# Optimization experiments

Hardware: AMD Instinct MI355X
Metric: run time of the kernel (lower is better)

## Reference

```python
import jax, jax.numpy as jnp
import numpy as np

B, H, W = 32, 480, 640
EPS = 1e-4


def _se3_exp(xi):
    """xi: [B,6] twist (v, w) -> (t [B,3], q [B,4] xyzw) of exp(xi)."""
    v, w = xi[:, :3], xi[:, 3:]
    theta2 = jnp.sum(w * w, axis=-1, keepdims=True)           # [B,1]
    theta = jnp.sqrt(theta2)
    small = theta < EPS
    safe_t = jnp.where(small, 1.0, theta)
    safe_t2 = jnp.where(small, 1.0, theta2)
    # quaternion: [sin(theta/2)/theta * w, cos(theta/2)], Taylor for small theta
    s_over = jnp.where(small, 0.5 - theta2 / 48.0, jnp.sin(0.5 * theta) / safe_t)
    q = jnp.concatenate([s_over * w, jnp.cos(0.5 * theta)], axis=-1)  # [B,4]
    # left Jacobian V = I + Bc*hat(w) + Cc*hat(w)^2
    Bc = jnp.where(small, 0.5 - theta2 / 24.0, (1.0 - jnp.cos(theta)) / safe_t2)
    Cc = jnp.where(small, 1.0 / 6.0 - theta2 / 120.0,
                   (theta - jnp.sin(theta)) / (safe_t2 * safe_t))
    wxv = jnp.cross(w, v)
    t = v + Bc * wxv + Cc * jnp.cross(w, wxv)                 # [B,3]
    return t, q


def _qmul(q1, q2):
    """Hamilton product, xyzw convention."""
    x1, y1, z1, w1 = jnp.split(q1, 4, axis=-1)
    x2, y2, z2, w2 = jnp.split(q2, 4, axis=-1)
    return jnp.concatenate([
        w1 * x2 + x1 * w2 + y1 * z2 - z1 * y2,
        w1 * y2 - x1 * z2 + y1 * w2 + z1 * x2,
        w1 * z2 + x1 * y2 - y1 * x2 + z1 * w2,
        w1 * w2 - x1 * x2 - y1 * y2 - z1 * z2,
    ], axis=-1)


def _qrot(q, v):
    """Rotate vectors v [B,3] by unit quaternions q [B,4] (xyzw)."""
    u, w = q[:, :3], q[:, 3:]
    uv = jnp.cross(u, v)
    return v + 2.0 * (w * uv + jnp.cross(u, uv))


def setup_inputs() -> dict:
    key = jax.random.key(0)
    ks = jax.random.split(key, 6)
    cp = jax.random.normal(ks[0], (B, 7), jnp.float32)
    qn = cp[:, 3:] / jnp.linalg.norm(cp[:, 3:], axis=-1, keepdims=True)
    curr_pose = jnp.concatenate([cp[:, :3], qn], axis=-1)
    curr_depth = 0.5 + 9.5 * jax.random.uniform(ks[1], (B, H, W), jnp.float32)
    delta_pose = 0.01 * jax.random.normal(ks[2], (B, 6), jnp.float32)
    delta_depth = jax.random.normal(ks[3], (B, H, W), jnp.float32)
    a_p = jax.random.uniform(ks[4], (B, 1), jnp.float32)
    a_d = jax.random.uniform(ks[5], (B, H, W), jnp.float32)
    return {"curr_pose": curr_pose, "curr_depth": curr_depth,
            "delta_pose": delta_pose, "delta_depth": delta_depth,
            "a_p": a_p, "a_d": a_d}


def reference(curr_pose, curr_depth, delta_pose, delta_depth, a_p, a_d):
    new_depth = jnp.maximum(curr_depth + a_d * delta_depth, 0.1)
    t_d, q_d = _se3_exp(a_p * delta_pose)
    t_c, q_c = curr_pose[:, :3], curr_pose[:, 3:]
    # compose: new_pose = delta_SE3 * curr_pose
    t_new = _qrot(q_d, t_c) + t_d
    q_new = _qmul(q_d, q_c)
    new_pose = jnp.concatenate([t_new, q_new], axis=-1)
    return (new_pose, new_depth)
```

## Files before the change

kernel.cpp:

```cpp
#include <hip/hip_runtime.h>
#include <math.h>

#define SE3_EPS 1e-4f

__global__ __launch_bounds__(256) void PoseDepthUpdater_fused_kernel(
    const float* __restrict__ curr_pose,
    const float* __restrict__ curr_depth,
    const float* __restrict__ delta_pose,
    const float* __restrict__ delta_depth,
    const float* __restrict__ a_p,
    const float* __restrict__ a_d,
    float* __restrict__ out_pose,
    float* __restrict__ out_depth,
    int Bn, long n)
{
    if (blockIdx.x == 0 && threadIdx.x < (unsigned)Bn) {
        int b = threadIdx.x;
        float ap = a_p[b];
        float v0 = ap * delta_pose[b*6+0];
        float v1 = ap * delta_pose[b*6+1];
        float v2 = ap * delta_pose[b*6+2];
        float w0 = ap * delta_pose[b*6+3];
        float w1 = ap * delta_pose[b*6+4];
        float w2 = ap * delta_pose[b*6+5];

        float theta2 = w0*w0 + w1*w1 + w2*w2;
        float theta  = sqrtf(theta2);
        bool  small  = theta < SE3_EPS;
        float safe_t  = small ? 1.0f : theta;
        float safe_t2 = small ? 1.0f : theta2;

        float s_over = small ? (0.5f - theta2 * (1.0f/48.0f))
                             : (sinf(0.5f*theta) / safe_t);
        float qx = s_over * w0, qy = s_over * w1, qz = s_over * w2;
        float qw = cosf(0.5f * theta);

        float Bc = small ? (0.5f - theta2 * (1.0f/24.0f))
                         : ((1.0f - cosf(theta)) / safe_t2);
        float Cc = small ? (1.0f/6.0f - theta2 * (1.0f/120.0f))
                         : ((theta - sinf(theta)) / (safe_t2 * safe_t));

        float cx = w1*v2 - w2*v1;
        float cy = w2*v0 - w0*v2;
        float cz = w0*v1 - w1*v0;
        float dx = w1*cz - w2*cy;
        float dy = w2*cx - w0*cz;
        float dz = w0*cy - w1*cx;

        float td0 = v0 + Bc*cx + Cc*dx;
        float td1 = v1 + Bc*cy + Cc*dy;
        float td2 = v2 + Bc*cz + Cc*dz;

        float tc0 = curr_pose[b*7+0], tc1 = curr_pose[b*7+1], tc2 = curr_pose[b*7+2];
        float qcx = curr_pose[b*7+3], qcy = curr_pose[b*7+4];
        float qcz = curr_pose[b*7+5], qcw = curr_pose[b*7+6];

        float uvx = qy*tc2 - qz*tc1;
        float uvy = qz*tc0 - qx*tc2;
        float uvz = qx*tc1 - qy*tc0;
        float uuvx = qy*uvz - qz*uvy;
        float uuvy = qz*uvx - qx*uvz;
        float uuvz = qx*uvy - qy*uvx;

        float tn0 = tc0 + 2.0f*(qw*uvx + uuvx) + td0;
        float tn1 = tc1 + 2.0f*(qw*uvy + uuvy) + td1;
        float tn2 = tc2 + 2.0f*(qw*uvz + uuvz) + td2;

        float nx = qw*qcx + qx*qcw + qy*qcz - qz*qcy;
        float ny = qw*qcy - qx*qcz + qy*qcw + qz*qcx;
        float nz = qw*qcz + qx*qcy - qy*qcx + qz*qcw;
        float nw = qw*qcw - qx*qcx - qy*qcy - qz*qcz;

        out_pose[b*7+0] = tn0;
        out_pose[b*7+1] = tn1;
        out_pose[b*7+2] = tn2;
        out_pose[b*7+3] = nx;
        out_pose[b*7+4] = ny;
        out_pose[b*7+5] = nz;
        out_pose[b*7+6] = nw;
    }

    long n4 = n >> 2;
    const float4* __restrict__ c4 = (const float4*)curr_depth;
    const float4* __restrict__ d4 = (const float4*)delta_depth;
    const float4* __restrict__ a4 = (const float4*)a_d;
    float4* __restrict__ o4 = (float4*)out_depth;

    long tid    = (long)blockIdx.x * blockDim.x + threadIdx.x;
    long stride = (long)gridDim.x * blockDim.x;

    for (long i = tid; i < n4; i += stride) {
        float4 c = c4[i];
        float4 d = d4[i];
        float4 a = a4[i];
        float4 r;
        r.x = fmaxf(fmaf(a.x, d.x, c.x), 0.1f);
        r.y = fmaxf(fmaf(a.y, d.y, c.y), 0.1f);
        r.z = fmaxf(fmaf(a.z, d.z, c.z), 0.1f);
        r.w = fmaxf(fmaf(a.w, d.w, c.w), 0.1f);
        o4[i] = r;
    }

    long tail_start = n4 << 2;
    for (long j = tail_start + tid; j < n; j += stride) {
        out_depth[j] = fmaxf(fmaf(a_d[j], delta_depth[j], curr_depth[j]), 0.1f);
    }
}

extern "C" void kernel_launch(void* const* d_in, const int* in_sizes, int n_in,
                              void* d_out, int out_size, void* d_ws, size_t ws_size,
                              hipStream_t stream) {
    const float* curr_pose   = (const float*)d_in[0];
    const float* curr_depth  = (const float*)d_in[1];
    const float* delta_pose  = (const float*)d_in[2];
    const float* delta_depth = (const float*)d_in[3];
    const float* a_p         = (const float*)d_in[4];
    const float* a_d         = (const float*)d_in[5];

    int  Bn = in_sizes[0] / 7;
    long n  = (long)in_sizes[1];

    float* out       = (float*)d_out;
    float* out_pose  = out;
    float* out_depth = out + (long)Bn * 7;

    const int block = 256;
    long n4 = n >> 2;
    int grid = (int)((n4 + block - 1) / block);
    if (grid > 2048) grid = 2048;
    if (grid < 1) grid = 1;

    PoseDepthUpdater_fused_kernel<<<grid, block, 0, stream>>>(
        curr_pose, curr_depth, delta_pose, delta_depth, a_p, a_d,
        out_pose, out_depth, Bn, n);
}
```

Baseline: 28.68 us.

## Replace grid-stride depth loop with 4x unrolled batched loads and nontemporal stores

Drops the grid-stride loop capped at 2048 blocks. Each thread now handles four float4 elements spaced a block apart, and the grid is sized to cover the whole array. All loads are issued before any compute to raise memory-level parallelism, and outputs use nontemporal stores to avoid polluting cache. This launches many more blocks (about 2400 for 2.46M float4s) and raises register use per thread.

```diff
diff --git a/kernel.cpp b/kernel.cpp
--- a/kernel.cpp
+++ b/kernel.cpp
@@ -2,6 +2,9 @@
 #include <math.h>
 
 #define SE3_EPS 1e-4f
+#define UNROLL 4
+
+typedef float f32x4 __attribute__((ext_vector_type(4)));
 
 __global__ __launch_bounds__(256) void PoseDepthUpdater_fused_kernel(
     const float* __restrict__ curr_pose,
@@ -81,29 +84,48 @@
     }
 
     long n4 = n >> 2;
-    const float4* __restrict__ c4 = (const float4*)curr_depth;
-    const float4* __restrict__ d4 = (const float4*)delta_depth;
-    const float4* __restrict__ a4 = (const float4*)a_d;
-    float4* __restrict__ o4 = (float4*)out_depth;
+    const f32x4* __restrict__ c4 = (const f32x4*)curr_depth;
+    const f32x4* __restrict__ d4 = (const f32x4*)delta_depth;
+    const f32x4* __restrict__ a4 = (const f32x4*)a_d;
+    f32x4* __restrict__ o4 = (f32x4*)out_depth;
 
-    long tid    = (long)blockIdx.x * blockDim.x + threadIdx.x;
-    long stride = (long)gridDim.x * blockDim.x;
+    long base = (long)blockIdx.x * (blockDim.x * UNROLL) + threadIdx.x;
 
-    for (long i = tid; i < n4; i += stride) {
-        float4 c = c4[i];
-        float4 d = d4[i];
-        float4 a = a4[i];
-        float4 r;
-        r.x = fmaxf(fmaf(a.x, d.x, c.x), 0.1f);
-        r.y = fmaxf(fmaf(a.y, d.y, c.y), 0.1f);
-        r.z = fmaxf(fmaf(a.z, d.z, c.z), 0.1f);
-        r.w = fmaxf(fmaf(a.w, d.w, c.w), 0.1f);
-        o4[i] = r;
+    long  idx[UNROLL];
+    bool  ok[UNROLL];
+    f32x4 c[UNROLL], d[UNROLL], a[UNROLL];
+
+    #pragma unroll
+    for (int k = 0; k < UNROLL; ++k) {
+        idx[k] = base + (long)k * blockDim.x;
+        ok[k]  = idx[k] < n4;
+    }
+    #pragma unroll
+    for (int k = 0; k < UNROLL; ++k) if (ok[k]) c[k] = c4[idx[k]];
+    #pragma unroll
+    for (int k = 0; k < UNROLL; ++k) if (ok[k]) d[k] = d4[idx[k]];
+    #pragma unroll
+    for (int k = 0; k < UNROLL; ++k) if (ok[k]) a[k] = a4[idx[k]];
+
+    #pragma unroll
+    for (int k = 0; k < UNROLL; ++k) {
+        if (ok[k]) {
+            f32x4 r;
+            r.x = fmaxf(fmaf(a[k].x, d[k].x, c[k].x), 0.1f);
+            r.y = fmaxf(fmaf(a[k].y, d[k].y, c[k].y), 0.1f);
+            r.z = fmaxf(fmaf(a[k].z, d[k].z, c[k].z), 0.1f);
+            r.w = fmaxf(fmaf(a[k].w, d[k].w, c[k].w), 0.1f);
+            __builtin_nontemporal_store(r, &o4[idx[k]]);
+        }
     }
 
     long tail_start = n4 << 2;
-    for (long j = tail_start + tid; j < n; j += stride) {
-        out_depth[j] = fmaxf(fmaf(a_d[j], delta_depth[j], curr_depth[j]), 0.1f);
+    if (tail_start < n) {
+        long tid    = (long)blockIdx.x * blockDim.x + threadIdx.x;
+        long stride = (long)gridDim.x * blockDim.x;
+        for (long j = tail_start + tid; j < n; j += stride) {
+            out_depth[j] = fmaxf(fmaf(a_d[j], delta_depth[j], curr_depth[j]), 0.1f);
+        }
     }
 }
 
@@ -126,8 +148,8 @@
 
     const int block = 256;
     long n4 = n >> 2;
-    int grid = (int)((n4 + block - 1) / block);
-    if (grid > 2048) grid = 2048;
+    long per_block = (long)block * UNROLL;
+    int grid = (int)((n4 + per_block - 1) / per_block);
     if (grid < 1) grid = 1;
 
     PoseDepthUpdater_fused_kernel<<<grid, block, 0, stream>>>(
```

Result: faster. 27.88 us (-2.8%).
